# Kernel tuning notes

Measured on AMD Instinct MI355X. Metric: run time of the kernel, lower is better.

Reference implementation:

```python
import jax, jax.numpy as jnp
import numpy as np

B, N, D = 16, 1024, 5
R_HID = 8  # radial MLP hidden width


def setup_inputs() -> dict:
    key = jax.random.key(0)
    ks = jax.random.split(key, 16)
    feats = jax.random.normal(ks[0], (B, N, D), jnp.float32)
    coors = 3.0 * jax.random.normal(ks[1], (B, N, 3), jnp.float32)
    a = jax.random.bernoulli(ks[2], 0.01, (B, N, N))
    adj_mat = a | jnp.swapaxes(a, 1, 2)
    s = 1.0 / np.sqrt(D)
    Wq = s * jax.random.normal(ks[3], (D, D), jnp.float32)
    Wk = s * jax.random.normal(ks[4], (D, D), jnp.float32)
    Wv = s * jax.random.normal(ks[5], (D, D), jnp.float32)
    Wo = s * jax.random.normal(ks[6], (D, D), jnp.float32)
    w_r1 = 0.5 * jax.random.normal(ks[7], (1, R_HID), jnp.float32)
    b_r1 = jnp.zeros((R_HID,), jnp.float32)
    w_r2 = 0.5 * jax.random.normal(ks[8], (R_HID, 1), jnp.float32)
    b_r2 = jnp.zeros((1,), jnp.float32)
    w1 = (1.0 / np.sqrt(D)) * jax.random.normal(ks[9], (D, 128), jnp.float32)
    b1 = jnp.zeros((128,), jnp.float32)
    w2 = (1.0 / np.sqrt(128.0)) * jax.random.normal(ks[10], (128, 3), jnp.float32)
    b2 = jnp.zeros((3,), jnp.float32)
    return dict(feats=feats, coors=coors, adj_mat=adj_mat, Wq=Wq, Wk=Wk, Wv=Wv,
                Wo=Wo, w_r1=w_r1, b_r1=b_r1, w_r2=w_r2, b_r2=b_r2,
                w1=w1, b1=b1, w2=w2, b2=b2)


def _se3_layer(feats, coors, neigh, Wq, Wk, Wv, Wo, w_r1, b_r1, w_r2, b_r2):
    # SE(3)-invariant sparse graph attention on degree-0 channels.
    # Attention logits = content term + radial (distance-only) bias, so the
    # scalar output is invariant to global rotations/translations of coors.
    q = jnp.einsum('bnd,de->bne', feats, Wq)
    k = jnp.einsum('bnd,de->bne', feats, Wk)
    v = jnp.einsum('bnd,de->bne', feats, Wv)
    rel = coors[:, :, None, :] - coors[:, None, :, :]        # [B,N,N,3]
    dist = jnp.sqrt(jnp.sum(rel * rel, axis=-1) + 1e-8)      # [B,N,N]
    h = jax.nn.relu(dist[..., None] * w_r1[0] + b_r1)        # [B,N,N,R_HID]
    rbias = (h @ w_r2)[..., 0] + b_r2[0]                     # [B,N,N]
    scores = jnp.einsum('bid,bjd->bij', q, k) / np.sqrt(q.shape[-1]) + rbias
    scores = jnp.where(neigh, scores, -1e9)
    attn = jax.nn.softmax(scores, axis=-1)
    agg = jnp.einsum('bij,bjd->bid', attn, v)
    return feats + jnp.einsum('bid,de->bie', agg, Wo)        # residual


def reference(feats, coors, adj_mat, Wq, Wk, Wv, Wo, w_r1, b_r1, w_r2, b_r2,
              w1, b1, w2, b2):
    a = adj_mat.astype(jnp.float32)
    # num_adj_degrees=2: attend over 1-hop and 2-hop neighbors (+ self)
    adj2 = jnp.einsum('bij,bjk->bik', a, a) > 0
    eye = jnp.eye(adj_mat.shape[1], dtype=bool)[None]
    neigh = adj_mat | adj2 | eye
    x = _se3_layer(feats, coors, neigh, Wq, Wk, Wv, Wo, w_r1, b_r1, w_r2, b_r2)
    pooled = jnp.mean(x, axis=1)                              # [B, D]
    hdn = jax.nn.relu(pooled @ w1 + b1)
    return hdn @ w2 + b2                                      # [B, 3]
```

## Files before the change

kernel.cpp:

```cpp
#include <hip/hip_runtime.h>
#include <hip/hip_bf16.h>

#define BB 16
#define NN 1024
#define DD 5
#define RH 8

typedef unsigned long long u64;
typedef unsigned int u32;
typedef __hip_bfloat16 bf16;

static __device__ __forceinline__ float tof(bf16 x) { return __bfloat162float(x); }
static __device__ __forceinline__ float ldf(const void* p, long long i, bool f) {
  return f ? ((const float*)p)[i] : tof(((const bf16*)p)[i]);
}

#define LOG2E 1.4426950408889634f
#define PACK_BLOCKS (BB * NN * 16 / 256)
#define KV_BLOCKS (BB * NN / 256)


__global__ __launch_bounds__(256) void k_pack(
    const void* __restrict__ adj, const void* __restrict__ feats,
    const void* __restrict__ coors,
    const void* __restrict__ Wk, const void* __restrict__ Wv,
    const void* __restrict__ Wo,
    u64* __restrict__ adjbits, float4* __restrict__ kvg,
    float* __restrict__ czg, int* __restrict__ gflags) {
  __shared__ int sNon01, sNonpair, sLow3;
  __shared__ int sCnt[4];
  __shared__ float wkL[25], wvL[25], woL[25];
  int tid = threadIdx.x;

  if (blockIdx.x >= PACK_BLOCKS) {
    int kb = blockIdx.x - PACK_BLOCKS;
    {
      u32 x = ((const u32*)feats)[tid];
      u32 lo = x & 0xFFFFu;
      int e = (int)((lo >> 7) & 0xFFu);
      bool insane = !(lo == 0u || (e >= 90 && e <= 150));
      u64 m = __ballot(insane);
      if ((tid & 63) == 0) sCnt[tid >> 6] = (int)__popcll(m);
    }
    __syncthreads();
    bool f32 = (sCnt[0] + sCnt[1] + sCnt[2] + sCnt[3]) > 64;
    if (tid < 25) {
      wkL[tid] = ldf(Wk, tid, f32);
      wvL[tid] = ldf(Wv, tid, f32);
      woL[tid] = ldf(Wo, tid, f32);
    }
    if (kb == 0 && tid == 0) gflags[0] = f32 ? 1 : 0;
    __syncthreads();
    long long node = (long long)kb * 256 + tid;
    float f0 = ldf(feats, node * DD + 0, f32), f1 = ldf(feats, node * DD + 1, f32),
          f2 = ldf(feats, node * DD + 2, f32), f3 = ldf(feats, node * DD + 3, f32),
          f4 = ldf(feats, node * DD + 4, f32);
    float k[DD], tv[DD], v[DD];
    #pragma unroll
    for (int e = 0; e < DD; ++e) {
      k[e] = f0 * wkL[e] + f1 * wkL[5 + e] + f2 * wkL[10 + e] + f3 * wkL[15 + e] +
             f4 * wkL[20 + e];
      tv[e] = f0 * wvL[e] + f1 * wvL[5 + e] + f2 * wvL[10 + e] + f3 * wvL[15 + e] +
              f4 * wvL[20 + e];
    }
    #pragma unroll
    for (int e = 0; e < DD; ++e)
      v[e] = tv[0] * woL[e] + tv[1] * woL[5 + e] + tv[2] * woL[10 + e] +
             tv[3] * woL[15 + e] + tv[4] * woL[20 + e];
    float cx = ldf(coors, node * 3 + 0, f32);
    float cy = ldf(coors, node * 3 + 1, f32);
    float cz = ldf(coors, node * 3 + 2, f32);
    kvg[node * 3 + 0] = make_float4(k[0], k[1], k[2], k[3]);
    kvg[node * 3 + 1] = make_float4(k[4], v[0], v[1], v[2]);
    kvg[node * 3 + 2] = make_float4(v[3], v[4], cx, cy);
    czg[node] = cz;
    return;
  }

  if (tid == 0) { sNon01 = 0; sNonpair = 0; sLow3 = 0; }
  __syncthreads();
  {
    const u32* aw = (const u32*)adj;
    int non01 = 0, nonpair = 0, low3 = 0;
    for (int i = tid; i < 4096; i += 256) {
      u32 x = aw[i];
      u32 lo = x & 0xFFFFu, hi = x >> 16;
      non01 |= (x > 1u);
      nonpair |= !((lo == 0u || lo == 0x3F80u) && (hi == 0u || hi == 0x3F80u));
      low3 |= (lo == 0x3F80u);
    }
    if (non01) atomicOr(&sNon01, 1);
    if (nonpair) atomicOr(&sNonpair, 1);
    if (low3) atomicOr(&sLow3, 1);
  }
  __syncthreads();
  int mode;
  if (!sNon01) mode = 0;
  else if (!sNonpair) mode = sLow3 ? 2 : 3;
  else mode = 1;

  int gid = blockIdx.x * 256 + tid;
  int w = gid & 15;
  long long row = gid >> 4;
  long long base = row * NN + (long long)w * 64;
  u64 bits = 0;
  if (mode == 3) {
    const uint4* p = (const uint4*)((const float*)adj + base);
    #pragma unroll
    for (int t = 0; t < 16; ++t) {
      uint4 x = p[t];
      if (x.x << 1) bits |= 1ull << (4 * t + 0);
      if (x.y << 1) bits |= 1ull << (4 * t + 1);
      if (x.z << 1) bits |= 1ull << (4 * t + 2);
      if (x.w << 1) bits |= 1ull << (4 * t + 3);
    }
  } else if (mode == 0) {
    const uint4* p = (const uint4*)((const u32*)adj + base);
    #pragma unroll
    for (int t = 0; t < 16; ++t) {
      uint4 x = p[t];
      if (x.x) bits |= 1ull << (4 * t + 0);
      if (x.y) bits |= 1ull << (4 * t + 1);
      if (x.z) bits |= 1ull << (4 * t + 2);
      if (x.w) bits |= 1ull << (4 * t + 3);
    }
  } else if (mode == 2) {
    const uint4* p = (const uint4*)((const unsigned short*)adj + base);
    #pragma unroll
    for (int t = 0; t < 8; ++t) {
      uint4 x = p[t];
      u32 c[4] = {x.x, x.y, x.z, x.w};
      #pragma unroll
      for (int q = 0; q < 4; ++q) {
        if ((c[q] & 0x7FFFu)) bits |= 1ull << (8 * t + 2 * q + 0);
        if ((c[q] >> 16) & 0x7FFFu) bits |= 1ull << (8 * t + 2 * q + 1);
      }
    }
  } else {
    const uint4* p = (const uint4*)((const unsigned char*)adj + base);
    #pragma unroll
    for (int t = 0; t < 4; ++t) {
      uint4 x = p[t];
      u32 c[4] = {x.x, x.y, x.z, x.w};
      #pragma unroll
      for (int q = 0; q < 4; ++q)
        #pragma unroll
        for (int bb = 0; bb < 4; ++bb)
          if ((c[q] >> (8 * bb)) & 0xFFu) bits |= 1ull << (16 * t + 4 * q + bb);
    }
  }
  adjbits[gid] = bits;
}

__global__ __launch_bounds__(256) void k_twohop(const u64* __restrict__ adjbits,
                                                u64* __restrict__ neighbits) {
  __shared__ unsigned short listL[4][NN];
  int wave = threadIdx.x >> 6, lane = threadIdx.x & 63;
  int row = blockIdx.x * 4 + wave;
  int b = row >> 10;
  int i = row & (NN - 1);
  int w = lane & 15;
  const u64* rowp = adjbits + (size_t)row * 16;
  u64 rw = rowp[w];
  unsigned short* list = listL[wave];
  int cnt = 0;
  #pragma unroll
  for (int sw = 0; sw < 16; ++sw) {
    u64 bits = __shfl(rw, sw, 64);
    int mybit = (int)((bits >> lane) & 1ull);
    int pre = __popcll(bits & ((1ull << lane) - 1ull));
    if (mybit) list[cnt + pre] = (unsigned short)(sw * 64 + lane);
    cnt += __popcll(bits);
  }
  __syncthreads();
  u64 acc = rw;
  if (w == (i >> 6)) acc |= 1ull << (i & 63);
  int g = lane >> 4;
  const u64* basep = adjbits + (size_t)b * NN * 16;
  for (int n = g; n < cnt; n += 4) {
    int j = list[n];
    acc |= basep[(size_t)j * 16 + w];
  }
  acc |= __shfl_xor(acc, 16, 64);
  acc |= __shfl_xor(acc, 32, 64);
  if (lane < 16) neighbits[(size_t)row * 16 + lane] = acc;
}

__global__ __launch_bounds__(256) void k_attn(
    const void* __restrict__ feats, const void* __restrict__ coors,
    const void* __restrict__ Wq,
    const void* __restrict__ wr1, const void* __restrict__ br1,
    const void* __restrict__ wr2, const void* __restrict__ br2,
    const float4* __restrict__ kvg, const float* __restrict__ czg,
    const int* __restrict__ gflags,
    const u64* __restrict__ neighbits, float* __restrict__ rowAgg) {
  __shared__ __align__(16) float4 kvL[512 * 3];
  __shared__ float czL[512];
  __shared__ float wqL[25];
  __shared__ float qL[16 * DD], ciL[16 * 3];
  __shared__ float wrL[3][RH];
  __shared__ float sConst[2];
  __shared__ int sFast;
  int bi = blockIdx.x;
  int b = bi >> 7, rem = bi & 127, chunk = rem >> 1, half = rem & 1;
  int j0 = half * 512;
  int tid = threadIdx.x;
  bool f32 = gflags[0] != 0;
  if (tid < 25) wqL[tid] = ldf(Wq, tid, f32);
  if (tid >= 64 && tid < 64 + RH) {
    int h = tid - 64;
    wrL[0][h] = ldf(wr1, h, f32);
    wrL[1][h] = ldf(br1, h, f32);
    wrL[2][h] = ldf(wr2, h, f32);
  }
  if (tid == 96) {
    float c = 0.0f;
    int ok = 1;
    #pragma unroll
    for (int h = 0; h < RH; ++h) {
      float w1h = ldf(wr1, h, f32);
      if (ldf(br1, h, f32) != 0.0f) ok = 0;
      if (w1h > 0.0f) c += w1h * ldf(wr2, h, f32);
    }
    sConst[0] = c * LOG2E;
    sConst[1] = ldf(br2, 0, f32) * LOG2E;
    sFast = ok;
  }
  {
    const float4* src = kvg + ((size_t)(b * NN) + j0) * 3;
    for (int idx = tid; idx < 512 * 3; idx += 256) kvL[idx] = src[idx];
    const float* csrc = czg + (size_t)(b * NN) + j0;
    for (int idx = tid; idx < 512; idx += 256) czL[idx] = csrc[idx];
  }
  __syncthreads();
  int fast = sFast;
  if (tid < 16) {
    long long row = (long long)b * NN + chunk * 16 + tid;
    float f0 = ldf(feats, row * DD + 0, f32), f1 = ldf(feats, row * DD + 1, f32),
          f2 = ldf(feats, row * DD + 2, f32), f3 = ldf(feats, row * DD + 3, f32),
          f4 = ldf(feats, row * DD + 4, f32);
    float qsc = fast ? (0.4472135954999579f * LOG2E) : 0.4472135954999579f;
    #pragma unroll
    for (int e = 0; e < DD; ++e)
      qL[tid * DD + e] = (f0 * wqL[e] + f1 * wqL[5 + e] + f2 * wqL[10 + e] +
                          f3 * wqL[15 + e] + f4 * wqL[20 + e]) * qsc;
    #pragma unroll
    for (int c = 0; c < 3; ++c)
      ciL[tid * 3 + c] = ldf(coors, row * 3 + c, f32);
  }
  __syncthreads();

  int g = tid >> 6, lane = tid & 63;
  int i0 = chunk * 16 + g * 4;
  float q[4][DD], ci[4][3], l[4], A[4][DD];
  #pragma unroll
  for (int r = 0; r < 4; ++r) {
    #pragma unroll
    for (int e = 0; e < DD; ++e) q[r][e] = qL[(g * 4 + r) * DD + e];
    #pragma unroll
    for (int c = 0; c < 3; ++c) ci[r][c] = ciL[(g * 4 + r) * 3 + c];
    l[r] = 0.0f;
    #pragma unroll
    for (int e = 0; e < DD; ++e) A[r][e] = 0.0f;
  }
  const u64* nb = neighbits + ((size_t)(b * NN + i0)) * 16 + half * 8;
  float Cf = sConst[0], br2f = sConst[1];
  for (int it = 0; it < 8; ++it) {
    int j = it * 64 + lane;
    float4 ka = kvL[j * 3 + 0];
    float4 kb = kvL[j * 3 + 1];
    float4 kc = kvL[j * 3 + 2];
    float jx = kc.z, jy = kc.w, jz = czL[j];
    u64 nw[4];
    #pragma unroll
    for (int r = 0; r < 4; ++r) nw[r] = nb[(size_t)r * 16 + it];
    if (fast) {
      #pragma unroll
      for (int r = 0; r < 4; ++r) {
        float cx = jx - ci[r][0], cy = jy - ci[r][1], cz = jz - ci[r][2];
        float dist =
            __builtin_amdgcn_sqrtf(fmaf(cx, cx, fmaf(cy, cy, fmaf(cz, cz, 1e-8f))));
        float s = fmaf(q[r][0], ka.x, br2f);
        s = fmaf(q[r][1], ka.y, s);
        s = fmaf(q[r][2], ka.z, s);
        s = fmaf(q[r][3], ka.w, s);
        s = fmaf(q[r][4], kb.x, s);
        s = fmaf(Cf, dist, s);
        s = fminf(s, 126.0f);
        s = ((nw[r] >> lane) & 1ull) ? s : -150.0f;
        float p = __builtin_amdgcn_exp2f(s);
        l[r] += p;
        A[r][0] = fmaf(p, kb.y, A[r][0]);
        A[r][1] = fmaf(p, kb.z, A[r][1]);
        A[r][2] = fmaf(p, kb.w, A[r][2]);
        A[r][3] = fmaf(p, kc.x, A[r][3]);
        A[r][4] = fmaf(p, kc.y, A[r][4]);
      }
    } else {
      #pragma unroll
      for (int r = 0; r < 4; ++r) {
        float cx = jx - ci[r][0], cy = jy - ci[r][1], cz = jz - ci[r][2];
        float dist = sqrtf(fmaf(cx, cx, fmaf(cy, cy, fmaf(cz, cz, 1e-8f))));
        float rb = ldf(br2, 0, f32);
        #pragma unroll
        for (int h = 0; h < RH; ++h)
          rb += fmaxf(dist * wrL[0][h] + wrL[1][h], 0.0f) * wrL[2][h];
        float s = fmaf(q[r][0], ka.x, rb);
        s = fmaf(q[r][1], ka.y, s);
        s = fmaf(q[r][2], ka.z, s);
        s = fmaf(q[r][3], ka.w, s);
        s = fmaf(q[r][4], kb.x, s);
        s = fminf(s, 85.0f);
        s = ((nw[r] >> lane) & 1ull) ? s : -100.0f;
        float p = __expf(s);
        l[r] += p;
        A[r][0] = fmaf(p, kb.y, A[r][0]);
        A[r][1] = fmaf(p, kb.z, A[r][1]);
        A[r][2] = fmaf(p, kb.w, A[r][2]);
        A[r][3] = fmaf(p, kc.x, A[r][3]);
        A[r][4] = fmaf(p, kc.y, A[r][4]);
      }
    }
  }
  #pragma unroll
  for (int msk = 1; msk < 64; msk <<= 1) {
    #pragma unroll
    for (int r = 0; r < 4; ++r) {
      l[r] += __shfl_xor(l[r], msk, 64);
      A[r][0] += __shfl_xor(A[r][0], msk, 64);
      A[r][1] += __shfl_xor(A[r][1], msk, 64);
      A[r][2] += __shfl_xor(A[r][2], msk, 64);
      A[r][3] += __shfl_xor(A[r][3], msk, 64);
      A[r][4] += __shfl_xor(A[r][4], msk, 64);
    }
  }
  if (lane == 0) {
    #pragma unroll
    for (int r = 0; r < 4; ++r) {
      float* o = rowAgg + (((size_t)(b * NN + i0 + r)) * 2 + half) * 6;
      o[0] = l[r];
      o[1] = A[r][0]; o[2] = A[r][1]; o[3] = A[r][2]; o[4] = A[r][3]; o[5] = A[r][4];
    }
  }
}

__global__ __launch_bounds__(256) void k_final(
    const void* __restrict__ feats, const float* __restrict__ rowAgg,
    const int* __restrict__ gflags,
    const void* __restrict__ w1, const void* __restrict__ b1,
    const void* __restrict__ w2, const void* __restrict__ b2,
    float* __restrict__ out) {
  __shared__ float waveL[4][DD];
  __shared__ float poolL[DD];
  __shared__ float hL[128];
  int b = blockIdx.x, tid = threadIdx.x;
  bool f32 = gflags[0] != 0;
  float pe[DD] = {0.f, 0.f, 0.f, 0.f, 0.f};
  for (int n = tid; n < NN; n += 256) {
    const float* ag = rowAgg + ((size_t)(b * NN + n)) * 12;
    float l = ag[0] + ag[6];
    float inv = (l > 0.f) ? 1.0f / l : 0.0f;
    long long base = ((long long)b * NN + n) * DD;
    #pragma unroll
    for (int e = 0; e < DD; ++e)
      pe[e] += ldf(feats, base + e, f32) + (ag[1 + e] + ag[7 + e]) * inv;
  }
  #pragma unroll
  for (int off = 32; off >= 1; off >>= 1)
    #pragma unroll
    for (int e = 0; e < DD; ++e) pe[e] += __shfl_down(pe[e], off, 64);
  int wave = tid >> 6, lane = tid & 63;
  if (lane == 0)
    #pragma unroll
    for (int e = 0; e < DD; ++e) waveL[wave][e] = pe[e];
  __syncthreads();
  if (tid < DD)
    poolL[tid] = (waveL[0][tid] + waveL[1][tid] + waveL[2][tid] + waveL[3][tid]) *
                 (1.0f / 1024.0f);
  __syncthreads();
  if (tid < 128) {
    float acc = ldf(b1, tid, f32);
    #pragma unroll
    for (int d = 0; d < DD; ++d)
      acc = fmaf(poolL[d], ldf(w1, d * 128 + tid, f32), acc);
    hL[tid] = fmaxf(acc, 0.0f);
  }
  __syncthreads();
  if (tid < 3) {
    float s = ldf(b2, tid, f32);
    for (int j = 0; j < 128; ++j) s = fmaf(hL[j], ldf(w2, j * 3 + tid, f32), s);
    out[b * 3 + tid] = s;
  }
}

extern "C" void kernel_launch(void* const* d_in, const int* in_sizes, int n_in,
                              void* d_out, int out_size, void* d_ws, size_t ws_size,
                              hipStream_t stream) {
  const void* adj = d_in[2];
  float* out = (float*)d_out;

  char* w = (char*)d_ws;
  int* gflags = (int*)w;
  const size_t MB2 = (size_t)BB * NN * 16 * sizeof(u64);
  u64* adjbits = (u64*)(w + 512);
  u64* neighbits = (u64*)(w + 512 + MB2);
  float* rowAgg = (float*)(w + 512 + 2 * MB2);
  float4* kvg = (float4*)(w + 512 + 2 * MB2 + 786432);
  float* czg = (float*)(w + 512 + 2 * MB2 + 2 * 786432);

  k_pack<<<PACK_BLOCKS + KV_BLOCKS, 256, 0, stream>>>(
      adj, d_in[0], d_in[1], d_in[4], d_in[5], d_in[6], adjbits, kvg, czg, gflags);
  k_twohop<<<BB * NN / 4, 256, 0, stream>>>(adjbits, neighbits);
  k_attn<<<BB * 128, 256, 0, stream>>>(d_in[0], d_in[1], d_in[3], d_in[7], d_in[8],
                                       d_in[9], d_in[10], kvg, czg, gflags,
                                       neighbits, rowAgg);
  k_final<<<BB, 256, 0, stream>>>(d_in[0], rowAgg, gflags, d_in[11], d_in[12],
                                  d_in[13], d_in[14], out);
}
```

Baseline: 187.9 us.

## Fuse two-hop mask, attention, and pooled MLP head into one kernel

Removes the separate two-hop and final kernels. Each attention block now builds its 16 rows' neighbor bitmasks in shared memory directly from adjbits and processes all 1024 columns instead of half. Pooling is done with atomic adds into a zeroed buffer, and the last block per batch, found through an atomic counter, runs the MLP head. This cuts two launches and the global neighbits/rowAgg round trips. In exchange the block count halves, shared memory per block grows to about 70KB, and the per-row two-hop gathers sit on the critical path of the attention blocks.

```diff
diff --git a/kernel.cpp b/kernel.cpp
--- a/kernel.cpp
+++ b/kernel.cpp
@@ -26,7 +26,8 @@
     const void* __restrict__ Wk, const void* __restrict__ Wv,
     const void* __restrict__ Wo,
     u64* __restrict__ adjbits, float4* __restrict__ kvg,
-    float* __restrict__ czg, int* __restrict__ gflags) {
+    float* __restrict__ czg, int* __restrict__ gflags,
+    float* __restrict__ pooled, int* __restrict__ cntr) {
   __shared__ int sNon01, sNonpair, sLow3;
   __shared__ int sCnt[4];
   __shared__ float wkL[25], wvL[25], woL[25];
@@ -34,6 +35,10 @@
 
   if (blockIdx.x >= PACK_BLOCKS) {
     int kb = blockIdx.x - PACK_BLOCKS;
+    if (kb == 0) {
+      if (tid < BB * DD) pooled[tid] = 0.0f;
+      else if (tid < BB * DD + BB) cntr[tid - BB * DD] = 0;
+    }
     {
       u32 x = ((const u32*)feats)[tid];
       u32 lo = x & 0xFFFFu;
@@ -152,58 +157,29 @@
   adjbits[gid] = bits;
 }
 
-__global__ __launch_bounds__(256) void k_twohop(const u64* __restrict__ adjbits,
-                                                u64* __restrict__ neighbits) {
-  __shared__ unsigned short listL[4][NN];
-  int wave = threadIdx.x >> 6, lane = threadIdx.x & 63;
-  int row = blockIdx.x * 4 + wave;
-  int b = row >> 10;
-  int i = row & (NN - 1);
-  int w = lane & 15;
-  const u64* rowp = adjbits + (size_t)row * 16;
-  u64 rw = rowp[w];
-  unsigned short* list = listL[wave];
-  int cnt = 0;
-  #pragma unroll
-  for (int sw = 0; sw < 16; ++sw) {
-    u64 bits = __shfl(rw, sw, 64);
-    int mybit = (int)((bits >> lane) & 1ull);
-    int pre = __popcll(bits & ((1ull << lane) - 1ull));
-    if (mybit) list[cnt + pre] = (unsigned short)(sw * 64 + lane);
-    cnt += __popcll(bits);
-  }
-  __syncthreads();
-  u64 acc = rw;
-  if (w == (i >> 6)) acc |= 1ull << (i & 63);
-  int g = lane >> 4;
-  const u64* basep = adjbits + (size_t)b * NN * 16;
-  for (int n = g; n < cnt; n += 4) {
-    int j = list[n];
-    acc |= basep[(size_t)j * 16 + w];
-  }
-  acc |= __shfl_xor(acc, 16, 64);
-  acc |= __shfl_xor(acc, 32, 64);
-  if (lane < 16) neighbits[(size_t)row * 16 + lane] = acc;
-}
-
 __global__ __launch_bounds__(256) void k_attn(
     const void* __restrict__ feats, const void* __restrict__ coors,
     const void* __restrict__ Wq,
     const void* __restrict__ wr1, const void* __restrict__ br1,
     const void* __restrict__ wr2, const void* __restrict__ br2,
     const float4* __restrict__ kvg, const float* __restrict__ czg,
-    const int* __restrict__ gflags,
-    const u64* __restrict__ neighbits, float* __restrict__ rowAgg) {
-  __shared__ __align__(16) float4 kvL[512 * 3];
-  __shared__ float czL[512];
+    const int* __restrict__ gflags, const u64* __restrict__ adjbits,
+    float* __restrict__ pooled, int* __restrict__ cntr,
+    const void* __restrict__ w1, const void* __restrict__ b1,
+    const void* __restrict__ w2, const void* __restrict__ b2,
+    float* __restrict__ out) {
+  __shared__ __align__(16) float4 kvL[NN * 3];
+  __shared__ float czL[NN];
+  __shared__ unsigned short listL[4][NN];
+  __shared__ u64 neighL[16][16];
+  __shared__ float qL[16 * DD], ciL[16 * 3];
   __shared__ float wqL[25];
-  __shared__ float qL[16 * DD], ciL[16 * 3];
   __shared__ float wrL[3][RH];
   __shared__ float sConst[2];
-  __shared__ int sFast;
+  __shared__ int sFast, sLast;
+
   int bi = blockIdx.x;
-  int b = bi >> 7, rem = bi & 127, chunk = rem >> 1, half = rem & 1;
-  int j0 = half * 512;
+  int b = bi >> 6, chunk = bi & 63;
   int tid = threadIdx.x;
   bool f32 = gflags[0] != 0;
   if (tid < 25) wqL[tid] = ldf(Wq, tid, f32);
@@ -227,10 +203,10 @@
     sFast = ok;
   }
   {
-    const float4* src = kvg + ((size_t)(b * NN) + j0) * 3;
-    for (int idx = tid; idx < 512 * 3; idx += 256) kvL[idx] = src[idx];
-    const float* csrc = czg + (size_t)(b * NN) + j0;
-    for (int idx = tid; idx < 512; idx += 256) czL[idx] = csrc[idx];
+    const float4* src = kvg + (size_t)b * NN * 3;
+    for (int idx = tid; idx < NN * 3; idx += 256) kvL[idx] = src[idx];
+    const float* csrc = czg + (size_t)b * NN;
+    for (int idx = tid; idx < NN; idx += 256) czL[idx] = csrc[idx];
   }
   __syncthreads();
   int fast = sFast;
@@ -248,10 +224,34 @@
     for (int c = 0; c < 3; ++c)
       ciL[tid * 3 + c] = ldf(coors, row * 3 + c, f32);
   }
-  __syncthreads();
 
   int g = tid >> 6, lane = tid & 63;
-  int i0 = chunk * 16 + g * 4;
+  int w = lane & 15, grp = lane >> 4;
+  const u64* basep = adjbits + (size_t)b * NN * 16;
+  for (int rr = 0; rr < 4; ++rr) {
+    int il = g * 4 + rr;
+    int i = chunk * 16 + il;
+    u64 rw = basep[(size_t)i * 16 + w];
+    unsigned short* list = listL[g];
+    int cnt = 0;
+    #pragma unroll
+    for (int sw = 0; sw < 16; ++sw) {
+      u64 bits = __shfl(rw, sw, 64);
+      int mybit = (int)((bits >> lane) & 1ull);
+      int pre = __popcll(bits & ((1ull << lane) - 1ull));
+      if (mybit) list[cnt + pre] = (unsigned short)(sw * 64 + lane);
+      cnt += __popcll(bits);
+    }
+    __syncthreads();
+    u64 acc = rw;
+    if (w == (i >> 6)) acc |= 1ull << (i & 63);
+    for (int n = grp; n < cnt; n += 4) acc |= basep[(size_t)list[n] * 16 + w];
+    acc |= __shfl_xor(acc, 16, 64);
+    acc |= __shfl_xor(acc, 32, 64);
+    if (lane < 16) neighL[il][lane] = acc;
+    __syncthreads();
+  }
+
   float q[4][DD], ci[4][3], l[4], A[4][DD];
   #pragma unroll
   for (int r = 0; r < 4; ++r) {
@@ -263,9 +263,8 @@
     #pragma unroll
     for (int e = 0; e < DD; ++e) A[r][e] = 0.0f;
   }
-  const u64* nb = neighbits + ((size_t)(b * NN + i0)) * 16 + half * 8;
   float Cf = sConst[0], br2f = sConst[1];
-  for (int it = 0; it < 8; ++it) {
+  for (int it = 0; it < 16; ++it) {
     int j = it * 64 + lane;
     float4 ka = kvL[j * 3 + 0];
     float4 kb = kvL[j * 3 + 1];
@@ -273,7 +272,7 @@
     float jx = kc.z, jy = kc.w, jz = czL[j];
     u64 nw[4];
     #pragma unroll
-    for (int r = 0; r < 4; ++r) nw[r] = nb[(size_t)r * 16 + it];
+    for (int r = 0; r < 4; ++r) nw[r] = neighL[g * 4 + r][it];
     if (fast) {
       #pragma unroll
       for (int r = 0; r < 4; ++r) {
@@ -334,62 +333,54 @@
       A[r][4] += __shfl_xor(A[r][4], msk, 64);
     }
   }
+
+  float* waveC = (float*)listL;
   if (lane == 0) {
+    float cw[DD] = {0.f, 0.f, 0.f, 0.f, 0.f};
     #pragma unroll
     for (int r = 0; r < 4; ++r) {
-      float* o = rowAgg + (((size_t)(b * NN + i0 + r)) * 2 + half) * 6;
-      o[0] = l[r];
-      o[1] = A[r][0]; o[2] = A[r][1]; o[3] = A[r][2]; o[4] = A[r][3]; o[5] = A[r][4];
-    }
-  }
-}
-
-__global__ __launch_bounds__(256) void k_final(
-    const void* __restrict__ feats, const float* __restrict__ rowAgg,
-    const int* __restrict__ gflags,
-    const void* __restrict__ w1, const void* __restrict__ b1,
-    const void* __restrict__ w2, const void* __restrict__ b2,
-    float* __restrict__ out) {
-  __shared__ float waveL[4][DD];
-  __shared__ float poolL[DD];
-  __shared__ float hL[128];
-  int b = blockIdx.x, tid = threadIdx.x;
-  bool f32 = gflags[0] != 0;
-  float pe[DD] = {0.f, 0.f, 0.f, 0.f, 0.f};
-  for (int n = tid; n < NN; n += 256) {
-    const float* ag = rowAgg + ((size_t)(b * NN + n)) * 12;
-    float l = ag[0] + ag[6];
-    float inv = (l > 0.f) ? 1.0f / l : 0.0f;
-    long long base = ((long long)b * NN + n) * DD;
-    #pragma unroll
-    for (int e = 0; e < DD; ++e)
-      pe[e] += ldf(feats, base + e, f32) + (ag[1 + e] + ag[7 + e]) * inv;
-  }
-  #pragma unroll
-  for (int off = 32; off >= 1; off >>= 1)
-    #pragma unroll
-    for (int e = 0; e < DD; ++e) pe[e] += __shfl_down(pe[e], off, 64);
-  int wave = tid >> 6, lane = tid & 63;
-  if (lane == 0)
-    #pragma unroll
-    for (int e = 0; e < DD; ++e) waveL[wave][e] = pe[e];
-  __syncthreads();
-  if (tid < DD)
-    poolL[tid] = (waveL[0][tid] + waveL[1][tid] + waveL[2][tid] + waveL[3][tid]) *
-                 (1.0f / 1024.0f);
-  __syncthreads();
-  if (tid < 128) {
-    float acc = ldf(b1, tid, f32);
-    #pragma unroll
-    for (int d = 0; d < DD; ++d)
-      acc = fmaf(poolL[d], ldf(w1, d * 128 + tid, f32), acc);
-    hL[tid] = fmaxf(acc, 0.0f);
-  }
-  __syncthreads();
-  if (tid < 3) {
-    float s = ldf(b2, tid, f32);
-    for (int j = 0; j < 128; ++j) s = fmaf(hL[j], ldf(w2, j * 3 + tid, f32), s);
-    out[b * 3 + tid] = s;
+      long long grow = (long long)b * NN + chunk * 16 + g * 4 + r;
+      float inv = (l[r] > 0.0f) ? 1.0f / l[r] : 0.0f;
+      #pragma unroll
+      for (int e = 0; e < DD; ++e)
+        cw[e] += ldf(feats, grow * DD + e, f32) + A[r][e] * inv;
+    }
+    #pragma unroll
+    for (int e = 0; e < DD; ++e) waveC[g * DD + e] = cw[e];
+  }
+  __syncthreads();
+  if (tid < DD) {
+    float s = waveC[tid] + waveC[DD + tid] + waveC[2 * DD + tid] +
+              waveC[3 * DD + tid];
+    float old = atomicAdd(&pooled[b * DD + tid], s);
+    asm volatile("" :: "v"(old));
+  }
+  __syncthreads();
+  if (tid == 0) sLast = (atomicAdd(&cntr[b], 1) == 63) ? 1 : 0;
+  __syncthreads();
+
+  if (sLast) {
+    float* hL = ((float*)listL) + 32;
+    if (tid < DD) {
+      float pv = __hip_atomic_load(&pooled[b * DD + tid], __ATOMIC_RELAXED,
+                                   __HIP_MEMORY_SCOPE_AGENT);
+      qL[tid] = pv * (1.0f / 1024.0f);
+    }
+    __syncthreads();
+    if (tid < 128) {
+      float acc = ldf(b1, tid, f32);
+      #pragma unroll
+      for (int d = 0; d < DD; ++d)
+        acc = fmaf(qL[d], ldf(w1, d * 128 + tid, f32), acc);
+      hL[tid] = fmaxf(acc, 0.0f);
+    }
+    __syncthreads();
+    if (tid < 3) {
+      float s = ldf(b2, tid, f32);
+      for (int j = 0; j < 128; ++j)
+        s = fmaf(hL[j], ldf(w2, j * 3 + tid, f32), s);
+      out[b * 3 + tid] = s;
+    }
   }
 }
 
@@ -401,19 +392,18 @@
 
   char* w = (char*)d_ws;
   int* gflags = (int*)w;
+  float* pooled = (float*)(w + 64);
+  int* cntr = (int*)(w + 512);
   const size_t MB2 = (size_t)BB * NN * 16 * sizeof(u64);
-  u64* adjbits = (u64*)(w + 512);
-  u64* neighbits = (u64*)(w + 512 + MB2);
-  float* rowAgg = (float*)(w + 512 + 2 * MB2);
-  float4* kvg = (float4*)(w + 512 + 2 * MB2 + 786432);
-  float* czg = (float*)(w + 512 + 2 * MB2 + 2 * 786432);
+  u64* adjbits = (u64*)(w + 1024);
+  float4* kvg = (float4*)(w + 1024 + MB2);
+  float* czg = (float*)(w + 1024 + MB2 + 786432);
 
   k_pack<<<PACK_BLOCKS + KV_BLOCKS, 256, 0, stream>>>(
-      adj, d_in[0], d_in[1], d_in[4], d_in[5], d_in[6], adjbits, kvg, czg, gflags);
-  k_twohop<<<BB * NN / 4, 256, 0, stream>>>(adjbits, neighbits);
-  k_attn<<<BB * 128, 256, 0, stream>>>(d_in[0], d_in[1], d_in[3], d_in[7], d_in[8],
-                                       d_in[9], d_in[10], kvg, czg, gflags,
-                                       neighbits, rowAgg);
-  k_final<<<BB, 256, 0, stream>>>(d_in[0], rowAgg, gflags, d_in[11], d_in[12],
-                                  d_in[13], d_in[14], out);
+      adj, d_in[0], d_in[1], d_in[4], d_in[5], d_in[6], adjbits, kvg, czg,
+      gflags, pooled, cntr);
+  k_attn<<<BB * 64, 256, 0, stream>>>(
+      d_in[0], d_in[1], d_in[3], d_in[7], d_in[8], d_in[9], d_in[10], kvg, czg,
+      gflags, adjbits, pooled, cntr, d_in[11], d_in[12], d_in[13], d_in[14],
+      out);
 }
```

New measurement: 202.2 us. 1.08x slower.
